# Kernel optimization log

Measured on AMD Instinct MI355X. Metric: run time of the kernel, lower is better.

The kernel has to match this reference:

```python
import jax, jax.numpy as jnp
from jax import lax
import numpy as np

IMGSIZE = (360, 640)  # (H, W)
SIGMA = 71.0
LEVEL = 5
FACTOR = 2.0

_k1 = np.array([1., 4., 6., 4., 1.], dtype=np.float32) / 16.0
K5 = np.outer(_k1, _k1)  # 5x5 binomial (Gaussian) pyramid kernel


def _blur(x, scale=1.0):
    # x: (B,C,H,W); depthwise 5x5 Gaussian blur with reflect padding
    C = x.shape[1]
    xp = jnp.pad(x, ((0, 0), (0, 0), (2, 2), (2, 2)), mode='reflect')
    k = jnp.broadcast_to(jnp.asarray(K5 * scale, x.dtype), (C, 1, 5, 5))
    return lax.conv_general_dilated(xp, k, (1, 1), 'VALID',
                                    feature_group_count=C,
                                    dimension_numbers=('NCHW', 'OIHW', 'NCHW'))


def pyrdown(x):
    # OpenCV-style pyrDown: blur then drop every other row/col -> ceil(H/2), ceil(W/2)
    return _blur(x)[:, :, ::2, ::2]


def pyrup(x):
    # OpenCV-style pyrUp: zero-insertion upsample then blur with 4*kernel
    B, C, H, W = x.shape
    up = jnp.zeros((B, C, 2 * H, 2 * W), x.dtype).at[:, :, ::2, ::2].set(x)
    return _blur(up, scale=4.0)


def resize_nearest(x, h, w):
    # matches torch F.interpolate(mode='nearest'): src = floor(dst * in/out)
    H, W = x.shape[-2], x.shape[-1]
    ri = jnp.arange(h) * H // h
    ci = jnp.arange(w) * W // w
    return x[..., ri[:, None], ci[None, :]]


def _create_filter(height, width, sigma):
    s = 2.0 * sigma * sigma
    xc = int(round(width * 0.5))
    yc = int(round(height * 0.5))
    ex = jnp.arange(-xc, width - xc - 1, dtype=jnp.float32)   # (W-1,)
    ey = jnp.arange(-yc, height - yc - 1, dtype=jnp.float32)  # (H-1,)
    d = ex[:, None] ** 2 + ey[None, :] ** 2                   # (W-1, H-1)
    g = jnp.exp(-d / s)
    return (g / g.max()).T                                    # (H-1, W-1)


def _pyramid_filters():
    f = _create_filter(int(FACTOR * IMGSIZE[0]), int(FACTOR * IMGSIZE[1]), SIGMA)
    filters = [f]
    for _ in range(LEVEL):
        filters.append(pyrdown(filters[-1][None, None])[0, 0])
    return filters


def setup_inputs():
    key = jax.random.key(0)
    k1, k2 = jax.random.split(key)
    B, C = 32, 3
    H, W = IMGSIZE
    images = jax.random.normal(k1, (B, C, H, W), jnp.float32)
    u = jax.random.uniform(k2, (B, 2), jnp.float32)
    # fixations are (x, y) pixel coordinates inside the image
    fixations = u * jnp.array([W - 1.0, H - 1.0], jnp.float32)
    return {"images": images, "fixations": fixations}


def reference(images, fixations):
    filters = _pyramid_filters()
    # Laplacian pyramid construction
    pyr, cur = [], images
    up = images
    for _ in range(LEVEL):
        dn = pyrdown(cur)
        up = resize_nearest(pyrup(dn), cur.shape[2], cur.shape[3])
        pyr.append(cur - up)
        cur = dn
    fovea = up  # smallest level, upsampled back (im_smallest)
    for i in range(LEVEL - 1, -1, -1):
        f = filters[i]
        fh, fw = f.shape
        ih, iw = pyr[i].shape[2], pyr[i].shape[3]
        fix = fixations / (2.0 ** i)
        # rect = filter_size/2 - fix, truncated to int (same as torch .to(int64))
        x1 = (fw / 2.0 - fix[:, 0]).astype(jnp.int32)
        y1 = (fh / 2.0 - fix[:, 1]).astype(jnp.int32)
        # per-sample dynamic crop of size (ih, iw); crop size == target size so
        # the original's F.interpolate on the crop is the identity
        crop = jax.vmap(lambda yy, xx: lax.dynamic_slice(f, (yy, xx), (ih, iw)))(y1, x1)
        filtered = pyr[i] * crop[:, None, :, :]
        if i != LEVEL - 1:
            fovea = resize_nearest(pyrup(fovea), ih, iw)
        fovea = fovea + filtered
    return fovea
```

## Files before the change

kernel.cpp:

```cpp
#include <hip/hip_runtime.h>
#include <cstddef>


static __device__ __forceinline__ int refl(int e, int n) {
  if (e < 0) e = -e;
  if (e >= n) e = 2 * n - 2 - e;
  return e;
}

static __device__ __forceinline__ float4 loadu4(const float* p) {
  float4 v; __builtin_memcpy(&v, p, sizeof(float4)); return v;
}

__global__ __launch_bounds__(256) void filt1d_k(float* __restrict__ fyg,
                                                float* __restrict__ fxg) {
  __shared__ float sy[1394];
  __shared__ float sx[2479];
  const int oy[5] = {0, 719, 1079, 1259, 1349};
  const int ny[5] = {719, 360, 180, 90, 45};
  const int ox[5] = {0, 1279, 1919, 2239, 2399};
  const int nx[5] = {1279, 640, 320, 160, 80};
  int tid = threadIdx.x;
  for (int i = tid; i < 719; i += 256) {
    float d = (float)(i - 360); sy[i] = expf(-d * d / 10082.0f);
  }
  for (int i = tid; i < 1279; i += 256) {
    float d = (float)(i - 640); sx[i] = expf(-d * d / 10082.0f);
  }
  __syncthreads();
  const float k0 = 0.0625f, k1 = 0.25f, k2 = 0.375f;
#pragma unroll
  for (int l = 1; l < 5; ++l) {
    const float* py = sy + oy[l - 1]; float* qy = sy + oy[l];
    int n = ny[l - 1];
    for (int i = tid; i < ny[l]; i += 256) {
      qy[i] = k0 * (py[refl(2 * i - 2, n)] + py[refl(2 * i + 2, n)]) +
              k1 * (py[refl(2 * i - 1, n)] + py[refl(2 * i + 1, n)]) +
              k2 * py[2 * i];
    }
    const float* px = sx + ox[l - 1]; float* qx = sx + ox[l];
    int m = nx[l - 1];
    for (int i = tid; i < nx[l]; i += 256) {
      qx[i] = k0 * (px[refl(2 * i - 2, m)] + px[refl(2 * i + 2, m)]) +
              k1 * (px[refl(2 * i - 1, m)] + px[refl(2 * i + 1, m)]) +
              k2 * px[2 * i];
    }
    __syncthreads();
  }
  for (int i = tid; i < 1394; i += 256) fyg[i] = sy[i];
  for (int i = tid; i < 2479; i += 256) fxg[i] = sx[i];
}

__global__ __launch_bounds__(256) void pyrdown_lds_k(
    const float* __restrict__ src, float* __restrict__ dst,
    int H, int W, int oH, int oW) {
  __shared__ float te[35][68];
  __shared__ float to_[35][68];
  int tx = threadIdx.x;
  int ty = threadIdx.y;
  int x0 = blockIdx.x * 64;
  int Yb = blockIdx.y;
  int p  = blockIdx.z;
  const float* s = src + (size_t)p * H * W;
  float* d = dst + (size_t)p * oH * oW;

  int cols = min(64, oW - x0);
  int nq   = (cols + 4) >> 1;
  int gr0  = 32 * Yb - 2;
  int gc0  = 2 * x0 - 4;
  int tid  = ty * 64 + tx;

  auto loadq = [&](int r, int m) -> float4 {
    int gy = refl(gr0 + r, H);
    const float* row = s + (size_t)gy * W;
    int gc = gc0 + 4 * m;
    if (gc >= 0 && gc + 3 < W) return *(const float4*)(row + gc);
    float4 v;
    v.x = row[refl(gc, W)];
    v.y = row[refl(gc + 1, W)];
    v.z = row[refl(gc + 2, W)];
    v.w = row[refl(gc + 3, W)];
    return v;
  };
  auto putq = [&](int r, int m, float4 v) {
    *(float2*)&te[r][2 * m]  = make_float2(v.x, v.z);
    *(float2*)&to_[r][2 * m] = make_float2(v.y, v.w);
  };

  if (nq == 34) {
    int r0 = tid / 34,          m0 = tid - 34 * r0;
    int q1 = tid + 256;  int r1 = q1 / 34, m1 = q1 - 34 * r1;
    int q2 = tid + 512;  int r2 = q2 / 34, m2 = q2 - 34 * r2;
    int q3 = tid + 768;  int r3 = q3 / 34, m3 = q3 - 34 * r3;
    int q4 = tid + 1024; int r4 = q4 / 34, m4 = q4 - 34 * r4;
    bool g4 = (q4 < 1190);
    float4 v0 = loadq(r0, m0);
    float4 v1 = loadq(r1, m1);
    float4 v2 = loadq(r2, m2);
    float4 v3 = loadq(r3, m3);
    float4 v4;
    if (g4) v4 = loadq(r4, m4);
    putq(r0, m0, v0);
    putq(r1, m1, v1);
    putq(r2, m2, v2);
    putq(r3, m3, v3);
    if (g4) putq(r4, m4, v4);
  } else {
    float4 v[9];
#pragma unroll
    for (int i = 0; i < 9; ++i) {
      int r = ty + 4 * i;
      if (r < 35 && tx < nq) v[i] = loadq(r, tx);
    }
#pragma unroll
    for (int i = 0; i < 9; ++i) {
      int r = ty + 4 * i;
      if (r < 35 && tx < nq) putq(r, tx, v[i]);
    }
  }
  __syncthreads();

  int x = x0 + tx;
  int nPairs = (oH + 1) >> 1;
  int Yp0 = 8 * Yb + 2 * ty;
  if (x < oW && Yp0 < nPairs) {
    const float k0 = 0.0625f, k1 = 0.25f, k2 = 0.375f;
    float h[11];
    int rbase = 8 * ty;
#pragma unroll
    for (int a = 0; a < 11; ++a) {
      int r = rbase + a;
      float e0 = te[r][tx + 1], e2 = te[r][tx + 2], e4 = te[r][tx + 3];
      float e1 = to_[r][tx + 1], e3 = to_[r][tx + 2];
      h[a] = k0 * (e0 + e4) + k1 * (e1 + e3) + k2 * e2;
    }
    float o0 = k0 * (h[0] + h[4])  + k1 * (h[1] + h[3])  + k2 * h[2];
    float o1 = k0 * (h[2] + h[6])  + k1 * (h[3] + h[5])  + k2 * h[4];
    float o2 = k0 * (h[4] + h[8])  + k1 * (h[5] + h[7])  + k2 * h[6];
    float o3 = k0 * (h[6] + h[10]) + k1 * (h[7] + h[9])  + k2 * h[8];
    int oy0 = 2 * Yp0;
    float* drow = d + (size_t)oy0 * oW + x;
    drow[0] = o0;
    if (oy0 + 1 < oH) drow[(size_t)oW] = o1;
    if (oy0 + 2 < oH) drow[(size_t)2 * oW] = o2;
    if (oy0 + 3 < oH) drow[(size_t)3 * oW] = o3;
  }
}

static __device__ __forceinline__ float pyrdown_at(const float* c, int H, int W,
                                                   int y, int x) {
  const float k0 = 0.0625f, k1 = 0.25f, k2 = 0.375f;
  int c0 = refl(2 * x - 2, W), c1 = refl(2 * x - 1, W), c2 = 2 * x,
      c3 = refl(2 * x + 1, W), c4 = refl(2 * x + 2, W);
  float h[5];
#pragma unroll
  for (int r = 0; r < 5; ++r) {
    int gy = refl(2 * y - 2 + r, H);
    const float* row = c + gy * W;
    h[r] = k0 * (row[c0] + row[c4]) + k1 * (row[c1] + row[c3]) + k2 * row[c2];
  }
  return k0 * (h[0] + h[4]) + k1 * (h[1] + h[3]) + k2 * h[2];
}

static __device__ __forceinline__ float pyrup_at(const float* c, int Hc, int Wc,
                                                 int y, int x) {
  const float w0 = 0.125f, w1 = 0.75f;
  int yc = y >> 1, xc = x >> 1;
  if (y & 1) {
    int yb = (yc == Hc - 1) ? Hc - 1 : yc + 1;
    const float* ra = c + yc * Wc;
    const float* rb = c + yb * Wc;
    if (x & 1) {
      int xb = (xc == Wc - 1) ? Wc - 1 : xc + 1;
      return 0.25f * (ra[xc] + ra[xb] + rb[xc] + rb[xb]);
    } else {
      int xm = (xc == 0) ? 1 : xc - 1, xp = (xc == Wc - 1) ? Wc - 1 : xc + 1;
      float a = w1 * ra[xc] + w0 * (ra[xm] + ra[xp]);
      float b = w1 * rb[xc] + w0 * (rb[xm] + rb[xp]);
      return 0.5f * (a + b);
    }
  } else {
    int ym = (yc == 0) ? 1 : yc - 1, yp = (yc == Hc - 1) ? Hc - 1 : yc + 1;
    const float* rm = c + ym * Wc;
    const float* rc = c + yc * Wc;
    const float* rp = c + yp * Wc;
    if (x & 1) {
      int xb = (xc == Wc - 1) ? Wc - 1 : xc + 1;
      float a = 0.5f * (rm[xc] + rm[xb]);
      float b = 0.5f * (rc[xc] + rc[xb]);
      float e = 0.5f * (rp[xc] + rp[xb]);
      return w1 * b + w0 * (a + e);
    } else {
      int xm = (xc == 0) ? 1 : xc - 1, xp = (xc == Wc - 1) ? Wc - 1 : xc + 1;
      float a = w1 * rm[xc] + w0 * (rm[xm] + rm[xp]);
      float b = w1 * rc[xc] + w0 * (rc[xm] + rc[xp]);
      float e = w1 * rp[xc] + w0 * (rp[xm] + rp[xp]);
      return w1 * b + w0 * (a + e);
    }
  }
}

__global__ __launch_bounds__(256) void tail_k(
    const float* __restrict__ dn3, const float* __restrict__ fix,
    const float* __restrict__ fy3, const float* __restrict__ fx3,
    const float* __restrict__ fy4, const float* __restrict__ fx4,
    float* __restrict__ fv3) {
  __shared__ float c3[45 * 80];
  __shared__ float c4[23 * 40];
  __shared__ float c5[12 * 20];
  __shared__ float g4[23 * 40];
  int p = blockIdx.x;
  int tid = threadIdx.x;
  const float* src = dn3 + (size_t)p * 3600;
  for (int i = tid; i < 900; i += 256)
    ((float4*)c3)[i] = ((const float4*)src)[i];
  __syncthreads();
  for (int i = tid; i < 23 * 40; i += 256) {
    int y = i / 40, x = i - 40 * y;
    c4[i] = pyrdown_at(c3, 45, 80, y, x);
  }
  __syncthreads();
  for (int i = tid; i < 12 * 20; i += 256) {
    int y = i / 20, x = i - 20 * y;
    c5[i] = pyrdown_at(c4, 23, 40, y, x);
  }
  __syncthreads();
  int b = p / 3;
  float fxv = fix[2 * b + 0], fyv = fix[2 * b + 1];
  {
    int x1 = (int)(40.0f - fxv * 0.0625f);
    int y1 = (int)(22.5f - fyv * 0.0625f);
    for (int i = tid; i < 23 * 40; i += 256) {
      int y = i / 40, x = i - 40 * y;
      float u = pyrup_at(c5, 12, 20, y, x);
      g4[i] = u + (c4[i] - u) * (fy4[y1 + y] * fx4[x1 + x]);
    }
  }
  __syncthreads();
  {
    int x1 = (int)(80.0f - fxv * 0.125f);
    int y1 = (int)(45.0f - fyv * 0.125f);
    float* dst = fv3 + (size_t)p * 3600;
    for (int i = tid; i < 45 * 80; i += 256) {
      int y = i / 80, x = i - 80 * y;
      float uf = pyrup_at(g4, 23, 40, y, x);
      float ud = pyrup_at(c4, 23, 40, y, x);
      dst[i] = uf + (c3[i] - ud) * (fy3[y1 + y] * fx3[x1 + x]);
    }
  }
}

__global__ __launch_bounds__(256) void recon4_k(
    const float* __restrict__ fprev, const float* __restrict__ dnext,
    int Hc, int Wc, const float* __restrict__ cur,
    const float* __restrict__ fyl, const float* __restrict__ fxl,
    int fh, int fw,
    const float* __restrict__ fix, float inv_scale,
    float* __restrict__ out, int ih, int iw) {
  int X2 = blockIdx.x * blockDim.x + threadIdx.x;
  int Y  = blockIdx.y * blockDim.y + threadIdx.y;
  int Wp = Wc >> 1;
  if (X2 >= Wp || Y >= Hc) return;
  int p = blockIdx.z;

  int ry[3];
  ry[0] = (Y == 0) ? 1 : Y - 1;
  ry[1] = Y;
  ry[2] = (Y == Hc - 1) ? Hc - 1 : Y + 1;
  int c0 = 2 * X2;
  const float* dn  = dnext + (size_t)p * Hc * Wc;
  const float* fpv = fprev + (size_t)p * Hc * Wc;
  bool two = (fprev != dnext);
  bool interior = (X2 >= 1) && (X2 <= Wp - 2);

  float dm[3], da[3], db[3], dq[3];
  float em[3], ea[3], eb[3], eq[3];
  if (interior) {
#pragma unroll
    for (int r = 0; r < 3; ++r) {
      const float* q = dn + (size_t)ry[r] * Wc + c0;
      float2 A = *(const float2*)(q - 2);
      float2 B = *(const float2*)(q);
      float2 C = *(const float2*)(q + 2);
      dm[r] = A.y; da[r] = B.x; db[r] = B.y; dq[r] = C.x;
    }
    if (two) {
#pragma unroll
      for (int r = 0; r < 3; ++r) {
        const float* q = fpv + (size_t)ry[r] * Wc + c0;
        float2 A = *(const float2*)(q - 2);
        float2 B = *(const float2*)(q);
        float2 C = *(const float2*)(q + 2);
        em[r] = A.y; ea[r] = B.x; eb[r] = B.y; eq[r] = C.x;
      }
    }
  } else {
    int cm = (c0 == 0) ? 1 : c0 - 1;
    int cp = (c0 + 2 >= Wc) ? (Wc - 1) : c0 + 2;
#pragma unroll
    for (int r = 0; r < 3; ++r) {
      const float* row = dn + (size_t)ry[r] * Wc;
      dm[r] = row[cm]; da[r] = row[c0]; db[r] = row[c0 + 1]; dq[r] = row[cp];
    }
    if (two) {
#pragma unroll
      for (int r = 0; r < 3; ++r) {
        const float* row = fpv + (size_t)ry[r] * Wc;
        em[r] = row[cm]; ea[r] = row[c0]; eb[r] = row[c0 + 1]; eq[r] = row[cp];
      }
    }
  }

  const float w0 = 0.125f, w1 = 0.75f;
  float heA[3], hoA[3], heB[3], hoB[3];
#pragma unroll
  for (int r = 0; r < 3; ++r) {
    heA[r] = w1 * da[r] + w0 * (dm[r] + db[r]);
    hoA[r] = 0.5f * (da[r] + db[r]);
    heB[r] = w1 * db[r] + w0 * (da[r] + dq[r]);
    hoB[r] = 0.5f * (db[r] + dq[r]);
  }
  float u00 = w1 * heA[1] + w0 * (heA[0] + heA[2]);
  float u01 = w1 * hoA[1] + w0 * (hoA[0] + hoA[2]);
  float u02 = w1 * heB[1] + w0 * (heB[0] + heB[2]);
  float u03 = w1 * hoB[1] + w0 * (hoB[0] + hoB[2]);
  float u10 = 0.5f * (heA[1] + heA[2]);
  float u11 = 0.5f * (hoA[1] + hoA[2]);
  float u12 = 0.5f * (heB[1] + heB[2]);
  float u13 = 0.5f * (hoB[1] + hoB[2]);

  float f00, f01, f02, f03, f10, f11, f12, f13;
  if (two) {
    float geA[3], goA[3], geB[3], goB[3];
#pragma unroll
    for (int r = 0; r < 3; ++r) {
      geA[r] = w1 * ea[r] + w0 * (em[r] + eb[r]);
      goA[r] = 0.5f * (ea[r] + eb[r]);
      geB[r] = w1 * eb[r] + w0 * (ea[r] + eq[r]);
      goB[r] = 0.5f * (eb[r] + eq[r]);
    }
    f00 = w1 * geA[1] + w0 * (geA[0] + geA[2]);
    f01 = w1 * goA[1] + w0 * (goA[0] + goA[2]);
    f02 = w1 * geB[1] + w0 * (geB[0] + geB[2]);
    f03 = w1 * goB[1] + w0 * (goB[0] + goB[2]);
    f10 = 0.5f * (geA[1] + geA[2]);
    f11 = 0.5f * (goA[1] + goA[2]);
    f12 = 0.5f * (geB[1] + geB[2]);
    f13 = 0.5f * (goB[1] + goB[2]);
  } else {
    f00 = u00; f01 = u01; f02 = u02; f03 = u03;
    f10 = u10; f11 = u11; f12 = u12; f13 = u13;
  }

  int b = p / 3;
  float fxv = fix[2 * b + 0] * inv_scale;
  float fyv = fix[2 * b + 1] * inv_scale;
  int x1 = (int)(0.5f * (float)fw - fxv);
  int y1 = (int)(0.5f * (float)fh - fyv);

  int oy = 2 * Y, ox = 4 * X2;
  const float* crow = cur + (size_t)p * ih * iw + (size_t)oy * iw + ox;
  float* orow = out + (size_t)p * ih * iw + (size_t)oy * iw + ox;

  const float* fyp = fyl + (y1 + oy);
  float fyA = fyp[0], fyB = fyp[1];
  float4 fxq = loadu4(fxl + (x1 + ox));

  float4 cv = *(const float4*)crow;
  float4 r0v;
  r0v.x = f00 + (cv.x - u00) * (fyA * fxq.x);
  r0v.y = f01 + (cv.y - u01) * (fyA * fxq.y);
  r0v.z = f02 + (cv.z - u02) * (fyA * fxq.z);
  r0v.w = f03 + (cv.w - u03) * (fyA * fxq.w);
  *(float4*)orow = r0v;
  if (oy + 1 < ih) {
    float4 cv1 = *(const float4*)(crow + iw);
    float4 r1v;
    r1v.x = f10 + (cv1.x - u10) * (fyB * fxq.x);
    r1v.y = f11 + (cv1.y - u11) * (fyB * fxq.y);
    r1v.z = f12 + (cv1.z - u12) * (fyB * fxq.z);
    r1v.w = f13 + (cv1.w - u13) * (fyB * fxq.w);
    *(float4*)(orow + iw) = r1v;
  }
}

extern "C" void kernel_launch(void* const* d_in, const int* in_sizes, int n_in,
                              void* d_out, int out_size, void* d_ws, size_t ws_size,
                              hipStream_t stream) {
  const float* images = (const float*)d_in[0];
  const float* fix    = (const float*)d_in[1];
  float* out = (float*)d_out;
  float* ws  = (float*)d_ws;

  const int P = 96;

  size_t off = 0;
  auto alloc = [&](size_t n) { float* p = ws + off; off += (n + 3) & ~(size_t)3; return p; };
  float* fyg = alloc(1394);
  float* fxg = alloc(2479);
  float* dn1 = alloc((size_t)P * 180 * 320);
  float* dn2 = alloc((size_t)P * 90 * 160);
  float* dn3 = alloc((size_t)P * 45 * 80);
  float* fv3 = alloc((size_t)P * 45 * 80);
  float* fv2 = alloc((size_t)P * 90 * 160);
  float* fv1 = alloc((size_t)P * 180 * 320);
  if (ws_size < off * sizeof(float)) return;

  dim3 blk(64, 4, 1);
  auto pgrd = [](int oW, int oH, int p) {
    int nPairs = (oH + 1) / 2;
    return dim3((unsigned)((oW + 63) / 64), (unsigned)((nPairs + 7) / 8), (unsigned)p);
  };
  auto grd = [](int tx, int ty, int p) {
    return dim3((unsigned)((tx + 63) / 64), (unsigned)((ty + 3) / 4), (unsigned)p);
  };

  filt1d_k<<<dim3(1), dim3(256), 0, stream>>>(fyg, fxg);

  pyrdown_lds_k<<<pgrd(320, 180, P), blk, 0, stream>>>(images, dn1, 360, 640, 180, 320);
  pyrdown_lds_k<<<pgrd(160, 90, P), blk, 0, stream>>>(dn1, dn2, 180, 320, 90, 160);
  pyrdown_lds_k<<<pgrd(80, 45, P), blk, 0, stream>>>(dn2, dn3, 90, 160, 45, 80);

  tail_k<<<dim3(P), dim3(256), 0, stream>>>(
      dn3, fix, fyg + 1259, fxg + 2239, fyg + 1349, fxg + 2399, fv3);

  recon4_k<<<grd(40, 45, P), blk, 0, stream>>>(
      fv3, dn3, 45, 80, dn2, fyg + 1079, fxg + 1919, 180, 320, fix, 0.25f,
      fv2, 90, 160);
  recon4_k<<<grd(80, 90, P), blk, 0, stream>>>(
      fv2, dn2, 90, 160, dn1, fyg + 719, fxg + 1279, 360, 640, fix, 0.5f,
      fv1, 180, 320);
  recon4_k<<<grd(160, 180, P), blk, 0, stream>>>(
      fv1, dn1, 180, 320, images, fyg, fxg, 719, 1279, fix, 1.0f,
      out, 360, 640);
}
```

Measured before the change: 249.7 us.

## Fuse three reconstruction levels into one tiled kernel, fold filter build into pyrdown

Replaces the three recon4_k launches with a single recon_fused_k that loads halo tiles of dn1/dn2/dn3/fv3 into LDS and rebuilds fv2 and fv1 tiles on chip before writing the full-resolution output. This drops the global writes and re-reads of the fv2 and fv1 intermediates and two kernel launches. The 1D filter-table build moves into an extra z-slice of the first pyrdown launch, removing the separate single-block kernel. The cost is redundant halo recomputation at each tile border, smaller per-block parallelism, and extra LDS use.

Result: faster. 233.3 us (-6.5%).

```diff
diff --git a/kernel.cpp b/kernel.cpp
--- a/kernel.cpp
+++ b/kernel.cpp
@@ -8,19 +8,23 @@
   return e;
 }
 
+static __device__ __forceinline__ int mapi(int i, int n) {
+  return i < 0 ? -i : (i >= n ? n - 1 : i);
+}
+
 static __device__ __forceinline__ float4 loadu4(const float* p) {
   float4 v; __builtin_memcpy(&v, p, sizeof(float4)); return v;
 }
 
-__global__ __launch_bounds__(256) void filt1d_k(float* __restrict__ fyg,
-                                                float* __restrict__ fxg) {
-  __shared__ float sy[1394];
-  __shared__ float sx[2479];
+static __device__ void filt_build(float* pool, float* __restrict__ fyg,
+                                  float* __restrict__ fxg) {
+  float* sy = pool;
+  float* sx = pool + 1394;
   const int oy[5] = {0, 719, 1079, 1259, 1349};
   const int ny[5] = {719, 360, 180, 90, 45};
   const int ox[5] = {0, 1279, 1919, 2239, 2399};
   const int nx[5] = {1279, 640, 320, 160, 80};
-  int tid = threadIdx.x;
+  int tid = threadIdx.y * 64 + threadIdx.x;
   for (int i = tid; i < 719; i += 256) {
     float d = (float)(i - 360); sy[i] = expf(-d * d / 10082.0f);
   }
@@ -53,14 +57,20 @@
 
 __global__ __launch_bounds__(256) void pyrdown_lds_k(
     const float* __restrict__ src, float* __restrict__ dst,
-    int H, int W, int oH, int oW) {
-  __shared__ float te[35][68];
-  __shared__ float to_[35][68];
+    int H, int W, int oH, int oW, int NP,
+    float* __restrict__ fyo, float* __restrict__ fxo) {
+  __shared__ float pool[35 * 68 * 2];
   int tx = threadIdx.x;
   int ty = threadIdx.y;
+  int p  = blockIdx.z;
+  if (p >= NP) {
+    if (blockIdx.x == 0 && blockIdx.y == 0 && fyo) filt_build(pool, fyo, fxo);
+    return;
+  }
+  float* te = pool;
+  float* to_ = pool + 35 * 68;
   int x0 = blockIdx.x * 64;
   int Yb = blockIdx.y;
-  int p  = blockIdx.z;
   const float* s = src + (size_t)p * H * W;
   float* d = dst + (size_t)p * oH * oW;
 
@@ -83,8 +93,8 @@
     return v;
   };
   auto putq = [&](int r, int m, float4 v) {
-    *(float2*)&te[r][2 * m]  = make_float2(v.x, v.z);
-    *(float2*)&to_[r][2 * m] = make_float2(v.y, v.w);
+    *(float2*)&te[r * 68 + 2 * m]  = make_float2(v.x, v.z);
+    *(float2*)&to_[r * 68 + 2 * m] = make_float2(v.y, v.w);
   };
 
   if (nq == 34) {
@@ -130,8 +140,9 @@
 #pragma unroll
     for (int a = 0; a < 11; ++a) {
       int r = rbase + a;
-      float e0 = te[r][tx + 1], e2 = te[r][tx + 2], e4 = te[r][tx + 3];
-      float e1 = to_[r][tx + 1], e3 = to_[r][tx + 2];
+      float e0 = te[r * 68 + tx + 1], e2 = te[r * 68 + tx + 2],
+            e4 = te[r * 68 + tx + 3];
+      float e1 = to_[r * 68 + tx + 1], e3 = to_[r * 68 + tx + 2];
       h[a] = k0 * (e0 + e4) + k1 * (e1 + e3) + k2 * e2;
     }
     float o0 = k0 * (h[0] + h[4])  + k1 * (h[1] + h[3])  + k2 * h[2];
@@ -200,6 +211,27 @@
   }
 }
 
+static __device__ __forceinline__ float pyrup_flat(
+    const float* t, int pitch, int yo, int xo, int y, int x) {
+  const float w0 = 0.125f, w1 = 0.75f;
+  int ys = (y >> 1) - yo, xs = (x >> 1) - xo;
+  const float* rc = t + ys * pitch + xs;
+  float h0, h1, h2;
+  if (x & 1) {
+    h1 = 0.5f * (rc[0] + rc[1]);
+    h2 = 0.5f * (rc[pitch] + rc[pitch + 1]);
+    if (y & 1) return 0.5f * (h1 + h2);
+    h0 = 0.5f * (rc[-pitch] + rc[-pitch + 1]);
+    return w1 * h1 + w0 * (h0 + h2);
+  } else {
+    h1 = w1 * rc[0] + w0 * (rc[-1] + rc[1]);
+    h2 = w1 * rc[pitch] + w0 * (rc[pitch - 1] + rc[pitch + 1]);
+    if (y & 1) return 0.5f * (h1 + h2);
+    h0 = w1 * rc[-pitch] + w0 * (rc[-pitch - 1] + rc[-pitch + 1]);
+    return w1 * h1 + w0 * (h0 + h2);
+  }
+}
+
 __global__ __launch_bounds__(256) void tail_k(
     const float* __restrict__ dn3, const float* __restrict__ fix,
     const float* __restrict__ fy3, const float* __restrict__ fx3,
@@ -250,65 +282,87 @@
   }
 }
 
-__global__ __launch_bounds__(256) void recon4_k(
-    const float* __restrict__ fprev, const float* __restrict__ dnext,
-    int Hc, int Wc, const float* __restrict__ cur,
-    const float* __restrict__ fyl, const float* __restrict__ fxl,
-    int fh, int fw,
-    const float* __restrict__ fix, float inv_scale,
-    float* __restrict__ out, int ih, int iw) {
-  int X2 = blockIdx.x * blockDim.x + threadIdx.x;
-  int Y  = blockIdx.y * blockDim.y + threadIdx.y;
-  int Wp = Wc >> 1;
-  if (X2 >= Wp || Y >= Hc) return;
-  int p = blockIdx.z;
-
-  int ry[3];
-  ry[0] = (Y == 0) ? 1 : Y - 1;
-  ry[1] = Y;
-  ry[2] = (Y == Hc - 1) ? Hc - 1 : Y + 1;
-  int c0 = 2 * X2;
-  const float* dn  = dnext + (size_t)p * Hc * Wc;
-  const float* fpv = fprev + (size_t)p * Hc * Wc;
-  bool two = (fprev != dnext);
-  bool interior = (X2 >= 1) && (X2 <= Wp - 2);
-
-  float dm[3], da[3], db[3], dq[3];
-  float em[3], ea[3], eb[3], eq[3];
-  if (interior) {
-#pragma unroll
-    for (int r = 0; r < 3; ++r) {
-      const float* q = dn + (size_t)ry[r] * Wc + c0;
-      float2 A = *(const float2*)(q - 2);
-      float2 B = *(const float2*)(q);
-      float2 C = *(const float2*)(q + 2);
-      dm[r] = A.y; da[r] = B.x; db[r] = B.y; dq[r] = C.x;
-    }
-    if (two) {
-#pragma unroll
-      for (int r = 0; r < 3; ++r) {
-        const float* q = fpv + (size_t)ry[r] * Wc + c0;
-        float2 A = *(const float2*)(q - 2);
-        float2 B = *(const float2*)(q);
-        float2 C = *(const float2*)(q + 2);
-        em[r] = A.y; ea[r] = B.x; eb[r] = B.y; eq[r] = C.x;
-      }
-    }
-  } else {
-    int cm = (c0 == 0) ? 1 : c0 - 1;
-    int cp = (c0 + 2 >= Wc) ? (Wc - 1) : c0 + 2;
-#pragma unroll
-    for (int r = 0; r < 3; ++r) {
-      const float* row = dn + (size_t)ry[r] * Wc;
-      dm[r] = row[cm]; da[r] = row[c0]; db[r] = row[c0 + 1]; dq[r] = row[cp];
-    }
-    if (two) {
-#pragma unroll
-      for (int r = 0; r < 3; ++r) {
-        const float* row = fpv + (size_t)ry[r] * Wc;
-        em[r] = row[cm]; ea[r] = row[c0]; eb[r] = row[c0 + 1]; eq[r] = row[cp];
-      }
-    }
+__global__ __launch_bounds__(256) void recon_fused_k(
+    const float* __restrict__ images, const float* __restrict__ dn1,
+    const float* __restrict__ dn2, const float* __restrict__ dn3,
+    const float* __restrict__ fv3g, const float* __restrict__ fyg,
+    const float* __restrict__ fxg, const float* __restrict__ fix,
+    float* __restrict__ out) {
+  __shared__ float fv1t[10 * 67];
+  __shared__ float dn1t[10 * 67];
+  __shared__ float fv2t[7 * 35];
+  __shared__ float dn2t[7 * 35];
+  __shared__ float fv3t[5 * 19];
+  __shared__ float dn3t[5 * 19];
+  const int bx = blockIdx.x, by = blockIdx.y, p = blockIdx.z;
+  const int tid = threadIdx.x;
+  const int R1o = 8 * by - 1, C1o = 64 * bx - 1;
+  const int R2o = 4 * by - 1, C2o = 32 * bx - 1;
+  const int R3o = 2 * by - 1, C3o = 16 * bx - 1;
+  const float* d1p = dn1 + (size_t)p * 57600;
+  const float* d2p = dn2 + (size_t)p * 14400;
+  const float* d3p = dn3 + (size_t)p * 3600;
+  const float* f3p = fv3g + (size_t)p * 3600;
+
+  for (int s = tid; s < 660; s += 256) {
+    int r = s / 66, c = s - 66 * r;
+    int gy = mapi(R1o + r, 180), gx = mapi(C1o + c, 320);
+    dn1t[r * 67 + c] = d1p[gy * 320 + gx];
+  }
+  if (tid < 245) {
+    int r = tid / 35, c = tid - 35 * r;
+    int gy = mapi(R2o + r, 90), gx = mapi(C2o + c, 160);
+    dn2t[tid] = d2p[gy * 160 + gx];
+  }
+  if (tid < 95) {
+    int r = tid / 19, c = tid - 19 * r;
+    int gy = mapi(R3o + r, 45), gx = mapi(C3o + c, 80);
+    dn3t[tid] = d3p[gy * 80 + gx];
+    fv3t[tid] = f3p[gy * 80 + gx];
+  }
+  __syncthreads();
+
+  int b = p / 3;
+  float fxv = fix[2 * b + 0], fyv = fix[2 * b + 1];
+  int y1_2 = (int)(90.0f - fyv * 0.25f), x1_2 = (int)(160.0f - fxv * 0.25f);
+  int y1_1 = (int)(180.0f - fyv * 0.5f), x1_1 = (int)(320.0f - fxv * 0.5f);
+  int y1_0 = (int)(359.5f - fyv),        x1_0 = (int)(639.5f - fxv);
+  const float* fy2 = fyg + 1079; const float* fx2 = fxg + 1919;
+  const float* fy1 = fyg + 719;  const float* fx1 = fxg + 1279;
+
+  if (tid < 245) {
+    int r = tid / 35, c = tid - 35 * r;
+    int gy = mapi(R2o + r, 90), gx = mapi(C2o + c, 160);
+    float uf = pyrup_flat(fv3t, 19, R3o, C3o, gy, gx);
+    float ud = pyrup_flat(dn3t, 19, R3o, C3o, gy, gx);
+    fv2t[tid] = uf + (dn2t[tid] - ud) * (fy2[y1_2 + gy] * fx2[x1_2 + gx]);
+  }
+  __syncthreads();
+
+  for (int s = tid; s < 660; s += 256) {
+    int r = s / 66, c = s - 66 * r;
+    int gy = mapi(R1o + r, 180), gx = mapi(C1o + c, 320);
+    float uf = pyrup_flat(fv2t, 35, R2o, C2o, gy, gx);
+    float ud = pyrup_flat(dn2t, 35, R2o, C2o, gy, gx);
+    fv1t[r * 67 + c] =
+        uf + (dn1t[r * 67 + c] - ud) * (fy1[y1_1 + gy] * fx1[x1_1 + gx]);
+  }
+  __syncthreads();
+
+  int trow = tid >> 5;
+  int tk   = tid & 31;
+  int Y = 8 * by + trow;
+  if (Y >= 180) return;
+  int c0 = 64 * bx + 2 * tk;
+  const float* dbase = dn1t + trow * 67 + 2 * tk;
+  const float* ebase = fv1t + trow * 67 + 2 * tk;
+  float dm[3], da[3], db[3], dq[3], em[3], ea[3], eb[3], eq[3];
+#pragma unroll
+  for (int r = 0; r < 3; ++r) {
+    const float* q = dbase + r * 67;
+    dm[r] = q[0]; da[r] = q[1]; db[r] = q[2]; dq[r] = q[3];
+    const float* e = ebase + r * 67;
+    em[r] = e[0]; ea[r] = e[1]; eb[r] = e[2]; eq[r] = e[3];
   }
 
   const float w0 = 0.125f, w1 = 0.75f;
@@ -329,42 +383,28 @@
   float u12 = 0.5f * (heB[1] + heB[2]);
   float u13 = 0.5f * (hoB[1] + hoB[2]);
 
-  float f00, f01, f02, f03, f10, f11, f12, f13;
-  if (two) {
-    float geA[3], goA[3], geB[3], goB[3];
-#pragma unroll
-    for (int r = 0; r < 3; ++r) {
-      geA[r] = w1 * ea[r] + w0 * (em[r] + eb[r]);
-      goA[r] = 0.5f * (ea[r] + eb[r]);
-      geB[r] = w1 * eb[r] + w0 * (ea[r] + eq[r]);
-      goB[r] = 0.5f * (eb[r] + eq[r]);
-    }
-    f00 = w1 * geA[1] + w0 * (geA[0] + geA[2]);
-    f01 = w1 * goA[1] + w0 * (goA[0] + goA[2]);
-    f02 = w1 * geB[1] + w0 * (geB[0] + geB[2]);
-    f03 = w1 * goB[1] + w0 * (goB[0] + goB[2]);
-    f10 = 0.5f * (geA[1] + geA[2]);
-    f11 = 0.5f * (goA[1] + goA[2]);
-    f12 = 0.5f * (geB[1] + geB[2]);
-    f13 = 0.5f * (goB[1] + goB[2]);
-  } else {
-    f00 = u00; f01 = u01; f02 = u02; f03 = u03;
-    f10 = u10; f11 = u11; f12 = u12; f13 = u13;
-  }
-
-  int b = p / 3;
-  float fxv = fix[2 * b + 0] * inv_scale;
-  float fyv = fix[2 * b + 1] * inv_scale;
-  int x1 = (int)(0.5f * (float)fw - fxv);
-  int y1 = (int)(0.5f * (float)fh - fyv);
-
-  int oy = 2 * Y, ox = 4 * X2;
-  const float* crow = cur + (size_t)p * ih * iw + (size_t)oy * iw + ox;
-  float* orow = out + (size_t)p * ih * iw + (size_t)oy * iw + ox;
-
-  const float* fyp = fyl + (y1 + oy);
-  float fyA = fyp[0], fyB = fyp[1];
-  float4 fxq = loadu4(fxl + (x1 + ox));
+  float geA[3], goA[3], geB[3], goB[3];
+#pragma unroll
+  for (int r = 0; r < 3; ++r) {
+    geA[r] = w1 * ea[r] + w0 * (em[r] + eb[r]);
+    goA[r] = 0.5f * (ea[r] + eb[r]);
+    geB[r] = w1 * eb[r] + w0 * (ea[r] + eq[r]);
+    goB[r] = 0.5f * (eb[r] + eq[r]);
+  }
+  float f00 = w1 * geA[1] + w0 * (geA[0] + geA[2]);
+  float f01 = w1 * goA[1] + w0 * (goA[0] + goA[2]);
+  float f02 = w1 * geB[1] + w0 * (geB[0] + geB[2]);
+  float f03 = w1 * goB[1] + w0 * (goB[0] + goB[2]);
+  float f10 = 0.5f * (geA[1] + geA[2]);
+  float f11 = 0.5f * (goA[1] + goA[2]);
+  float f12 = 0.5f * (geB[1] + geB[2]);
+  float f13 = 0.5f * (goB[1] + goB[2]);
+
+  int oy = 2 * Y, ox = 2 * c0;
+  const float* crow = images + (size_t)p * 230400 + (size_t)oy * 640 + ox;
+  float* orow = out + (size_t)p * 230400 + (size_t)oy * 640 + ox;
+  float fyA = fyg[y1_0 + oy], fyB = fyg[y1_0 + oy + 1];
+  float4 fxq = loadu4(fxg + (x1_0 + ox));
 
   float4 cv = *(const float4*)crow;
   float4 r0v;
@@ -373,15 +413,13 @@
   r0v.z = f02 + (cv.z - u02) * (fyA * fxq.z);
   r0v.w = f03 + (cv.w - u03) * (fyA * fxq.w);
   *(float4*)orow = r0v;
-  if (oy + 1 < ih) {
-    float4 cv1 = *(const float4*)(crow + iw);
-    float4 r1v;
-    r1v.x = f10 + (cv1.x - u10) * (fyB * fxq.x);
-    r1v.y = f11 + (cv1.y - u11) * (fyB * fxq.y);
-    r1v.z = f12 + (cv1.z - u12) * (fyB * fxq.z);
-    r1v.w = f13 + (cv1.w - u13) * (fyB * fxq.w);
-    *(float4*)(orow + iw) = r1v;
-  }
+  float4 cv1 = *(const float4*)(crow + 640);
+  float4 r1v;
+  r1v.x = f10 + (cv1.x - u10) * (fyB * fxq.x);
+  r1v.y = f11 + (cv1.y - u11) * (fyB * fxq.y);
+  r1v.z = f12 + (cv1.z - u12) * (fyB * fxq.z);
+  r1v.w = f13 + (cv1.w - u13) * (fyB * fxq.w);
+  *(float4*)(orow + 640) = r1v;
 }
 
 extern "C" void kernel_launch(void* const* d_in, const int* in_sizes, int n_in,
@@ -402,8 +440,6 @@
   float* dn2 = alloc((size_t)P * 90 * 160);
   float* dn3 = alloc((size_t)P * 45 * 80);
   float* fv3 = alloc((size_t)P * 45 * 80);
-  float* fv2 = alloc((size_t)P * 90 * 160);
-  float* fv1 = alloc((size_t)P * 180 * 320);
   if (ws_size < off * sizeof(float)) return;
 
   dim3 blk(64, 4, 1);
@@ -411,26 +447,17 @@
     int nPairs = (oH + 1) / 2;
     return dim3((unsigned)((oW + 63) / 64), (unsigned)((nPairs + 7) / 8), (unsigned)p);
   };
-  auto grd = [](int tx, int ty, int p) {
-    return dim3((unsigned)((tx + 63) / 64), (unsigned)((ty + 3) / 4), (unsigned)p);
-  };
-
-  filt1d_k<<<dim3(1), dim3(256), 0, stream>>>(fyg, fxg);
-
-  pyrdown_lds_k<<<pgrd(320, 180, P), blk, 0, stream>>>(images, dn1, 360, 640, 180, 320);
-  pyrdown_lds_k<<<pgrd(160, 90, P), blk, 0, stream>>>(dn1, dn2, 180, 320, 90, 160);
-  pyrdown_lds_k<<<pgrd(80, 45, P), blk, 0, stream>>>(dn2, dn3, 90, 160, 45, 80);
+
+  pyrdown_lds_k<<<pgrd(320, 180, P + 1), blk, 0, stream>>>(
+      images, dn1, 360, 640, 180, 320, P, fyg, fxg);
+  pyrdown_lds_k<<<pgrd(160, 90, P), blk, 0, stream>>>(
+      dn1, dn2, 180, 320, 90, 160, P, nullptr, nullptr);
+  pyrdown_lds_k<<<pgrd(80, 45, P), blk, 0, stream>>>(
+      dn2, dn3, 90, 160, 45, 80, P, nullptr, nullptr);
 
   tail_k<<<dim3(P), dim3(256), 0, stream>>>(
       dn3, fix, fyg + 1259, fxg + 2239, fyg + 1349, fxg + 2399, fv3);
 
-  recon4_k<<<grd(40, 45, P), blk, 0, stream>>>(
-      fv3, dn3, 45, 80, dn2, fyg + 1079, fxg + 1919, 180, 320, fix, 0.25f,
-      fv2, 90, 160);
-  recon4_k<<<grd(80, 90, P), blk, 0, stream>>>(
-      fv2, dn2, 90, 160, dn1, fyg + 719, fxg + 1279, 360, 640, fix, 0.5f,
-      fv1, 180, 320);
-  recon4_k<<<grd(160, 180, P), blk, 0, stream>>>(
-      fv1, dn1, 180, 320, images, fyg, fxg, 719, 1279, fix, 1.0f,
-      out, 360, 640);
-}
+  recon_fused_k<<<dim3(5, 23, P), dim3(256), 0, stream>>>(
+      images, dn1, dn2, dn3, fv3, fyg, fxg, fix, out);
+}
```
